# Performance work log

Measured on AMD Instinct MI355X. Metric: run time of the kernel, lower is better.

## Reference

```python
import jax, jax.numpy as jnp
import numpy as np

B, IN, FS, S, H = 4096, 4096, 4096, 64, 512  # batch, input_size, first_size, shape_lstm, n_hidden
D = FS // S  # per-step feature for left/right (=64); up/down per-step feature = S (=64)


def _lstm_cell(x, h, c, Wih, Whh, bih, bhh):
    # standard torch LSTMCell gate order: i, f, g, o
    g = x @ Wih.T + bih + h @ Whh.T + bhh  # (B, 4H)
    i, f, gg, o = jnp.split(g, 4, axis=-1)
    c = jax.nn.sigmoid(f) * c + jax.nn.sigmoid(i) * jnp.tanh(gg)
    h = jax.nn.sigmoid(o) * jnp.tanh(c)
    return h, c


def setup_inputs() -> dict:
    key = jax.random.key(0)
    ks = jax.random.split(key, 20)
    def cell(k, d_in):
        k1, k2, k3, k4 = jax.random.split(k, 4)
        s = 1.0 / np.sqrt(H)
        return (jax.random.uniform(k1, (4 * H, d_in), jnp.float32, -s, s),
                jax.random.uniform(k2, (4 * H, H), jnp.float32, -s, s),
                jax.random.uniform(k3, (4 * H,), jnp.float32, -s, s),
                jax.random.uniform(k4, (4 * H,), jnp.float32, -s, s))
    Wih_l, Whh_l, bih_l, bhh_l = cell(ks[0], D)
    Wih_r, Whh_r, bih_r, bhh_r = cell(ks[1], D)
    Wih_d, Whh_d, bih_d, bhh_d = cell(ks[2], S)
    return {
        "x": jax.random.normal(ks[3], (B, IN), jnp.float32),
        "h0": jax.random.normal(ks[4], (4, B, H), jnp.float32),
        "c0": jax.random.normal(ks[5], (4, B, H), jnp.float32),
        "W1": jax.random.normal(ks[6], (FS, IN), jnp.float32) * (1.0 / np.sqrt(IN)),
        "b1": jnp.zeros((FS,), jnp.float32),
        "Wih_l": Wih_l, "Whh_l": Whh_l, "bih_l": bih_l, "bhh_l": bhh_l,
        "Wih_r": Wih_r, "Whh_r": Whh_r, "bih_r": bih_r, "bhh_r": bhh_r,
        "Wih_d": Wih_d, "Whh_d": Whh_d, "bih_d": bih_d, "bhh_d": bhh_d,
        "W3": jax.random.normal(ks[7], (10, 4 * H), jnp.float32) * (1.0 / np.sqrt(4 * H)),
        "b3": jnp.zeros((10,), jnp.float32),
    }


def reference(x, h0, c0, W1, b1, Wih_l, Whh_l, bih_l, bhh_l,
              Wih_r, Whh_r, bih_r, bhh_r, Wih_d, Whh_d, bih_d, bhh_d, W3, b3):
    feat = jax.nn.relu(x @ W1.T + b1)            # (B, FS); dropout=identity (eval)
    il = feat.reshape(B, S, D)
    x_left = jnp.transpose(il, (1, 0, 2))         # (S, B, D)
    x_right = x_left[::-1]
    x_up = jnp.transpose(il, (2, 0, 1))           # (D, B, S); loop uses first S steps
    x_down = x_up[::-1]

    def step(carry, xs):
        (hl, cl, hr, cr, hu, cu, hd, cd) = carry
        xl, xr, xu, xd = xs
        hl, cl = _lstm_cell(xl, hl, cl, Wih_l, Whh_l, bih_l, bhh_l)
        hr, cr = _lstm_cell(xr, hr, cr, Wih_r, Whh_r, bih_r, bhh_r)
        # original code uses the DOWN cell for both up and down directions
        hu, cu = _lstm_cell(xu, hu, cu, Wih_d, Whh_d, bih_d, bhh_d)
        hd, cd = _lstm_cell(xd, hd, cd, Wih_d, Whh_d, bih_d, bhh_d)
        return (hl, cl, hr, cr, hu, cu, hd, cd), None

    carry0 = (h0[0], c0[0], h0[1], c0[1], h0[2], c0[2], h0[3], c0[3])
    (hl, _, hr, _, hu, _, hd, _), _ = jax.lax.scan(
        step, carry0, (x_left[:S], x_right[:S], x_up[:S], x_down[:S]))
    out = jnp.concatenate([hl, hr, hu, hd], axis=1)  # (B, 4H)
    logits = out @ W3.T + b3
    return jax.nn.log_softmax(logits, axis=1)
```

## Files before the change

kernel.cpp:

```cpp
#include <hip/hip_runtime.h>
#include <cstddef>
#include <cstdint>

namespace {

constexpr int kB  = 4096;
constexpr int kIN = 4096;
constexpr int kFS = 4096;
constexpr int kS  = 64;
constexpr int kH  = 512;
constexpr int kNG = 2048;
constexpr int kKC = 576;

typedef __bf16 bf16_t;
typedef __bf16 bfrag  __attribute__((ext_vector_type(8)));
typedef __bf16 bf16v4 __attribute__((ext_vector_type(4)));
typedef float  f32x4  __attribute__((ext_vector_type(4)));

__device__ __forceinline__ void gload16(const void* g, void* l) {
  __builtin_amdgcn_global_load_lds(
      (const __attribute__((address_space(1))) void*)g,
      (__attribute__((address_space(3))) void*)l, 16, 0, 0);
}

__device__ __forceinline__ float sigf(float x) { return 1.0f / (1.0f + __expf(-x)); }
__device__ __forceinline__ float tanh_fast(float x) {
  float e = __expf(2.0f * x);
  return 1.0f - 2.0f / (e + 1.0f);
}

__device__ __forceinline__ f32x4 mfma16(bfrag a, bfrag b, f32x4 c) {
  return __builtin_amdgcn_mfma_f32_16x16x32_bf16(a, b, c, 0, 0, 0);
}

__device__ __forceinline__ void vwait(const int n) {
  if (n == 6)      asm volatile("s_waitcnt vmcnt(6)" ::: "memory");
  else if (n == 4) asm volatile("s_waitcnt vmcnt(4)" ::: "memory");
  else             asm volatile("s_waitcnt vmcnt(0)" ::: "memory");
  __builtin_amdgcn_sched_barrier(0);
}


__global__ __launch_bounds__(256) void f2b4_kernel(const float* __restrict__ in,
                                                   bf16_t* __restrict__ out, int n4) {
  int i = blockIdx.x * 256 + threadIdx.x;
  if (i >= n4) return;
  float4 v = reinterpret_cast<const float4*>(in)[i];
  bf16v4 o = {(bf16_t)v.x, (bf16_t)v.y, (bf16_t)v.z, (bf16_t)v.w};
  *reinterpret_cast<bf16v4*>(out + (size_t)i * 4) = o;
}

__global__ __launch_bounds__(256) void pack_wcat_kernel(
    const float* __restrict__ Wih_l, const float* __restrict__ Whh_l,
    const float* __restrict__ Wih_r, const float* __restrict__ Whh_r,
    const float* __restrict__ Wih_d, const float* __restrict__ Whh_d,
    bf16_t* __restrict__ wcat) {
  int idx = blockIdx.x * 256 + threadIdx.x;
  if (idx >= 3 * kNG * kKC) return;
  int m = idx / (kNG * kKC);
  int rem = idx - m * (kNG * kKC);
  int rr = rem / kKC;
  int k  = rem - rr * kKC;
  int u = rr >> 2, g = rr & 3;
  int orow = g * kH + u;
  const float* Wih = (m == 0) ? Wih_l : (m == 1) ? Wih_r : Wih_d;
  const float* Whh = (m == 0) ? Whh_l : (m == 1) ? Whh_r : Whh_d;
  float v = (k < 64) ? Wih[(size_t)orow * 64 + k] : Whh[(size_t)orow * 512 + (k - 64)];
  wcat[idx] = (bf16_t)v;
}

__global__ __launch_bounds__(256) void pack_bias_kernel(
    const float* __restrict__ bih_l, const float* __restrict__ bhh_l,
    const float* __restrict__ bih_r, const float* __restrict__ bhh_r,
    const float* __restrict__ bih_d, const float* __restrict__ bhh_d,
    float* __restrict__ biasc) {
  int idx = blockIdx.x * 256 + threadIdx.x;
  if (idx >= 3 * kNG) return;
  int m = idx / kNG;
  int rr = idx - m * kNG;
  int u = rr >> 2, g = rr & 3;
  int orow = g * kH + u;
  const float* bi = (m == 0) ? bih_l : (m == 1) ? bih_r : bih_d;
  const float* bh = (m == 0) ? bhh_l : (m == 1) ? bhh_r : bhh_d;
  biasc[idx] = bi[orow] + bh[orow];
}

__global__ __launch_bounds__(256) void pack_hc_kernel(const float* __restrict__ h0,
                                                      const float* __restrict__ c0,
                                                      bf16_t* __restrict__ hbuf0,
                                                      float* __restrict__ cbuf, int n) {
  int i = blockIdx.x * 256 + threadIdx.x;
  if (i >= n) return;
  hbuf0[i] = (bf16_t)h0[i];
  cbuf[i]  = c0[i];
}

__global__ __launch_bounds__(256) void transpose64_kernel(const bf16_t* __restrict__ feat,
                                                          bf16_t* __restrict__ featT) {
  __shared__ bf16_t tile[64][65];
  const int b = blockIdx.x;
  const bf16_t* src = feat + (size_t)b * kFS;
  bf16_t* dst = featT + (size_t)b * kFS;
  for (int i = threadIdx.x; i < 4096; i += 256) tile[i >> 6][i & 63] = src[i];
  __syncthreads();
  for (int i = threadIdx.x; i < 4096; i += 256) dst[i] = tile[i & 63][i >> 6];
}


__global__ __launch_bounds__(256, 4) void gemm_feat_kernel(
    const bf16_t* __restrict__ X, const bf16_t* __restrict__ W,
    const float* __restrict__ b1, bf16_t* __restrict__ feat) {
  __shared__ bf16_t As[128 * 32];
  __shared__ bf16_t Bs[128 * 32];
  const int t = threadIdx.x;
  const int bid = blockIdx.x;
  const int widx = (bid & 7) * 128 + (bid >> 3);
  const int bm = widx & 31, bn = widx >> 5;
  const int w = t >> 6, l = t & 63;
  const int wm = (w >> 1) * 64, wn = (w & 1) * 64;
  const int sr = t >> 2;
  const int skS = ((t & 3) ^ ((t >> 3) & 3)) * 8;
  const int lr = l & 15;
  const int lkS = ((l >> 4) ^ ((l >> 1) & 3)) * 8;
  const int lrow4 = (l >> 4) * 4;

  f32x4 acc[4][4];
#pragma unroll
  for (int i = 0; i < 4; ++i)
#pragma unroll
    for (int j = 0; j < 4; ++j) acc[i][j] = (f32x4){0.f, 0.f, 0.f, 0.f};

  const bf16_t* ga = X + (size_t)(bm * 128 + sr) * kIN + skS;
  const bf16_t* gb = W + (size_t)(bn * 128 + sr) * kIN + skS;
  bf16_t* lA = As + w * 512;
  bf16_t* lB = Bs + w * 512;

  for (int kt = 0; kt < kIN / 32; ++kt) {
    gload16(ga, lA);
    gload16(ga + (size_t)64 * kIN, lA + 2048);
    gload16(gb, lB);
    gload16(gb + (size_t)64 * kIN, lB + 2048);
    ga += 32; gb += 32;
    __syncthreads();
    bfrag a[4], b[4];
#pragma unroll
    for (int mi = 0; mi < 4; ++mi)
      a[mi] = *reinterpret_cast<const bfrag*>(&As[(wm + mi * 16 + lr) * 32 + lkS]);
#pragma unroll
    for (int ni = 0; ni < 4; ++ni)
      b[ni] = *reinterpret_cast<const bfrag*>(&Bs[(wn + ni * 16 + lr) * 32 + lkS]);
#pragma unroll
    for (int mi = 0; mi < 4; ++mi)
#pragma unroll
      for (int ni = 0; ni < 4; ++ni)
        acc[mi][ni] = __builtin_amdgcn_mfma_f32_16x16x32_bf16(a[mi], b[ni], acc[mi][ni], 0, 0, 0);
    __syncthreads();
  }

#pragma unroll
  for (int ni = 0; ni < 4; ++ni) {
    const int col = bn * 128 + wn + ni * 16 + lr;
    const float bb = b1[col];
#pragma unroll
    for (int mi = 0; mi < 4; ++mi) {
#pragma unroll
      for (int r = 0; r < 4; ++r) {
        const int row = bm * 128 + wm + mi * 16 + lrow4 + r;
        float v = acc[mi][ni][r] + bb;
        feat[(size_t)row * kFS + col] = (bf16_t)fmaxf(v, 0.0f);
      }
    }
  }
}


template <class F1, class F2, class F3, class F4>
__device__ __forceinline__ void run_tile(
    const bf16_t* __restrict__ As_, const bf16_t* __restrict__ Bs_,
    f32x4 (&acc)[8][4], const int wr, const int wc, const int lr, const int lq,
    F1&& st1, F2&& st2, F3&& st3, F4&& st4,
    const int v1, const int v2, const int v3, const int v4) {
  bfrag a[8], b[8];
  const int sx = lr & 7;

#pragma unroll
  for (int mm = 0; mm < 4; ++mm)
#pragma unroll
    for (int kk = 0; kk < 2; ++kk)
      a[mm * 2 + kk] = *reinterpret_cast<const bfrag*>(
          As_ + (wr * 128 + mm * 16 + lr) * 64 + (((kk * 4 + lq) ^ sx) * 8));
#pragma unroll
  for (int nn = 0; nn < 2; ++nn)
#pragma unroll
    for (int kk = 0; kk < 2; ++kk)
      b[nn * 2 + kk] = *reinterpret_cast<const bfrag*>(
          Bs_ + (wc * 64 + nn * 16 + lr) * 64 + (((kk * 4 + lq) ^ sx) * 8));
  st1();
  __builtin_amdgcn_s_barrier();
  asm volatile("s_waitcnt lgkmcnt(0)" ::: "memory");
  __builtin_amdgcn_sched_barrier(0);
  __builtin_amdgcn_s_setprio(1);
#pragma unroll
  for (int kk = 0; kk < 2; ++kk)
#pragma unroll
    for (int mm = 0; mm < 4; ++mm)
#pragma unroll
      for (int nn = 0; nn < 2; ++nn)
        acc[mm][nn] = mfma16(a[mm * 2 + kk], b[nn * 2 + kk], acc[mm][nn]);
  __builtin_amdgcn_s_setprio(0);
  __builtin_amdgcn_sched_barrier(0);
  vwait(v1);
  __builtin_amdgcn_s_barrier();

#pragma unroll
  for (int nn = 0; nn < 2; ++nn)
#pragma unroll
    for (int kk = 0; kk < 2; ++kk)
      b[4 + nn * 2 + kk] = *reinterpret_cast<const bfrag*>(
          Bs_ + (wc * 64 + 32 + nn * 16 + lr) * 64 + (((kk * 4 + lq) ^ sx) * 8));
  st2();
  __builtin_amdgcn_s_barrier();
  asm volatile("s_waitcnt lgkmcnt(0)" ::: "memory");
  __builtin_amdgcn_sched_barrier(0);
  __builtin_amdgcn_s_setprio(1);
#pragma unroll
  for (int kk = 0; kk < 2; ++kk)
#pragma unroll
    for (int mm = 0; mm < 4; ++mm)
#pragma unroll
      for (int nn = 0; nn < 2; ++nn)
        acc[mm][2 + nn] = mfma16(a[mm * 2 + kk], b[4 + nn * 2 + kk], acc[mm][2 + nn]);
  __builtin_amdgcn_s_setprio(0);
  __builtin_amdgcn_sched_barrier(0);
  vwait(v2);
  __builtin_amdgcn_s_barrier();

#pragma unroll
  for (int mm = 0; mm < 4; ++mm)
#pragma unroll
    for (int kk = 0; kk < 2; ++kk)
      a[mm * 2 + kk] = *reinterpret_cast<const bfrag*>(
          As_ + (wr * 128 + 64 + mm * 16 + lr) * 64 + (((kk * 4 + lq) ^ sx) * 8));
  st3();
  __builtin_amdgcn_s_barrier();
  asm volatile("s_waitcnt lgkmcnt(0)" ::: "memory");
  __builtin_amdgcn_sched_barrier(0);
  __builtin_amdgcn_s_setprio(1);
#pragma unroll
  for (int kk = 0; kk < 2; ++kk)
#pragma unroll
    for (int mm = 0; mm < 4; ++mm)
#pragma unroll
      for (int nn = 0; nn < 2; ++nn)
        acc[4 + mm][nn] = mfma16(a[mm * 2 + kk], b[nn * 2 + kk], acc[4 + mm][nn]);
  __builtin_amdgcn_s_setprio(0);
  __builtin_amdgcn_sched_barrier(0);
  vwait(v3);
  __builtin_amdgcn_s_barrier();

  st4();
  __builtin_amdgcn_s_barrier();
  asm volatile("s_waitcnt lgkmcnt(0)" ::: "memory");
  __builtin_amdgcn_sched_barrier(0);
  __builtin_amdgcn_s_setprio(1);
#pragma unroll
  for (int kk = 0; kk < 2; ++kk)
#pragma unroll
    for (int mm = 0; mm < 4; ++mm)
#pragma unroll
      for (int nn = 0; nn < 2; ++nn)
        acc[4 + mm][2 + nn] = mfma16(a[mm * 2 + kk], b[4 + nn * 2 + kk], acc[4 + mm][2 + nn]);
  __builtin_amdgcn_s_setprio(0);
  __builtin_amdgcn_sched_barrier(0);
  vwait(v4);
  __builtin_amdgcn_s_barrier();
}

__global__ __launch_bounds__(512, 2) void lstm_step256_kernel(
    const bf16_t* __restrict__ feat, const bf16_t* __restrict__ featT,
    const bf16_t* __restrict__ wcat, const float* __restrict__ biasc,
    const bf16_t* __restrict__ hin, bf16_t* __restrict__ hout,
    float* __restrict__ cbuf, int s) {
  extern __shared__ __align__(16) char smem[];
  bf16_t* Ab[2] = {(bf16_t*)smem, (bf16_t*)(smem + 65536)};
  bf16_t* Bb[2] = {(bf16_t*)(smem + 32768), (bf16_t*)(smem + 98304)};

  const int t = threadIdx.x;
  const int l = t & 63, w = t >> 6;
  const int wr = w >> 2, wc = w & 3;
  const int lr = l & 15, lq = l >> 4;
  const int srow = l >> 3;
  const int sslot = (l & 7) ^ srow;

  const int bid = blockIdx.x;
  const int widx = (bid & 7) * 64 + (bid >> 3);
  const int cell = widx >> 7;
  const int rwk = widx & 127;
  const int bm = rwk >> 3, bn = rwk & 7;

  const bf16_t* xsrc = (cell < 2) ? feat : featT;
  const int off = ((cell & 1) ? (63 - s) : s) * 64;
  const int mat = (cell < 2) ? cell : 2;
  const bf16_t* Wm = wcat + (size_t)mat * kNG * kKC;
  const bf16_t* hc = hin + (size_t)cell * kB * kH;

  auto stage_A = [&](int kt, bf16_t* dstA, int ra) {
#pragma unroll
    for (int j = 0; j < 2; ++j) {
      const int row0 = ra * 64 + w * 8 + j * 128;
      bf16_t* dst = dstA + row0 * 64;
      const bf16_t* src = (kt == 0)
          ? xsrc + (size_t)(bm * 256 + row0 + srow) * kFS + off + sslot * 8
          : hc + (size_t)(bm * 256 + row0 + srow) * kH + (kt - 1) * 64 + sslot * 8;
      gload16(src, dst);
    }
  };
  auto stage_B = [&](int kt, bf16_t* dstB, int rb) {
#pragma unroll
    for (int j = 0; j < 2; ++j) {
      const int row0 = (w >> 2) * 64 + (w & 3) * 8 + rb * 32 + j * 128;
      bf16_t* dst = dstB + row0 * 64;
      const bf16_t* src =
          Wm + (size_t)(bn * 256 + row0 + srow) * kKC + kt * 64 + sslot * 8;
      gload16(src, dst);
    }
  };

  f32x4 acc[8][4];
#pragma unroll
  for (int i = 0; i < 8; ++i)
#pragma unroll
    for (int j = 0; j < 4; ++j) acc[i][j] = (f32x4){0.f, 0.f, 0.f, 0.f};

  stage_A(0, Ab[0], 0); stage_B(0, Bb[0], 0);
  stage_A(0, Ab[0], 1); stage_B(0, Bb[0], 1);
  stage_A(1, Ab[1], 0); stage_B(1, Bb[1], 0);
  vwait(4);
  __builtin_amdgcn_s_barrier();

  run_tile(Ab[0], Bb[0], acc, wr, wc, lr, lq,
           [&] { stage_A(1, Ab[1], 1); }, [&] { stage_B(1, Bb[1], 1); },
           [&] { stage_A(2, Ab[0], 0); }, [&] { stage_B(2, Bb[0], 0); },
           6, 6, 6, 6);

  for (int S = 1; S <= 5; S += 2) {
    run_tile(Ab[1], Bb[1], acc, wr, wc, lr, lq,
             [&] { stage_A(S + 1, Ab[0], 1); }, [&] { stage_B(S + 1, Bb[0], 1); },
             [&] { stage_A(S + 2, Ab[1], 0); }, [&] { stage_B(S + 2, Bb[1], 0); },
             6, 6, 6, 6);
    run_tile(Ab[0], Bb[0], acc, wr, wc, lr, lq,
             [&] { stage_A(S + 2, Ab[1], 1); }, [&] { stage_B(S + 2, Bb[1], 1); },
             [&] { stage_A(S + 3, Ab[0], 0); }, [&] { stage_B(S + 3, Bb[0], 0); },
             6, 6, 6, 6);
  }
  run_tile(Ab[1], Bb[1], acc, wr, wc, lr, lq,
           [&] { stage_A(8, Ab[0], 1); }, [&] { stage_B(8, Bb[0], 1); },
           [&] {}, [&] {}, 6, 6, 6, 4);
  run_tile(Ab[0], Bb[0], acc, wr, wc, lr, lq,
           [&] {}, [&] {}, [&] {}, [&] {}, 0, 0, 0, 0);

  float* Gw = (float*)smem + w * 2176;
  const float* biasn = biasc + mat * kNG + bn * 256 + wc * 64;
  float bb[4];
#pragma unroll
  for (int n = 0; n < 4; ++n) bb[n] = biasn[n * 16 + lr];
  const int rowg0 = bm * 256 + wr * 128;
  const int unit = bn * 64 + wc * 16 + lr;
#pragma unroll
  for (int ch = 0; ch < 4; ++ch) {
#pragma unroll
    for (int mm = 0; mm < 2; ++mm) {
      const int m = ch * 2 + mm;
#pragma unroll
      for (int n = 0; n < 4; ++n)
#pragma unroll
        for (int j = 0; j < 4; ++j)
          Gw[(mm * 16 + lq * 4 + j) * 68 + n * 16 + lr] = acc[m][n][j] + bb[n];
    }
#pragma unroll
    for (int rr = 0; rr < 8; ++rr) {
      const int row = rr * 4 + lq;
      const float4 g4 = *reinterpret_cast<const float4*>(&Gw[row * 68 + lr * 4]);
      const float iv = sigf(g4.x);
      const float fv = sigf(g4.y);
      const float gv = tanh_fast(g4.z);
      const float ov = sigf(g4.w);
      const int grow = rowg0 + ch * 32 + row;
      const size_t cidx = ((size_t)cell * kB + grow) * kH + unit;
      const float cn = fv * cbuf[cidx] + iv * gv;
      cbuf[cidx] = cn;
      hout[cidx] = (bf16_t)(ov * tanh_fast(cn));
    }
  }
}


__global__ __launch_bounds__(256) void head_kernel(const bf16_t* __restrict__ hfin,
                                                   const float* __restrict__ W3,
                                                   const float* __restrict__ b3,
                                                   float* __restrict__ out) {
  const int b = blockIdx.x, t = threadIdx.x;
  float acc[10];
#pragma unroll
  for (int j = 0; j < 10; ++j) acc[j] = 0.f;
  for (int k = t; k < 2048; k += 256) {
    const int cell = k >> 9, u = k & 511;
    const float hv = (float)hfin[((size_t)cell * kB + b) * kH + u];
#pragma unroll
    for (int j = 0; j < 10; ++j) acc[j] += hv * W3[j * 2048 + k];
  }
  __shared__ float red[256];
  __shared__ float logits[10];
  for (int j = 0; j < 10; ++j) {
    red[t] = acc[j];
    __syncthreads();
    for (int o2 = 128; o2 > 0; o2 >>= 1) {
      if (t < o2) red[t] += red[t + o2];
      __syncthreads();
    }
    if (t == 0) logits[j] = red[0] + b3[j];
    __syncthreads();
  }
  if (t == 0) {
    float mx = logits[0];
    for (int j = 1; j < 10; ++j) mx = fmaxf(mx, logits[j]);
    float se = 0.f;
    for (int j = 0; j < 10; ++j) se += expf(logits[j] - mx);
    const float lse = mx + logf(se);
    for (int j = 0; j < 10; ++j) out[(size_t)b * 10 + j] = logits[j] - lse;
  }
}

}

extern "C" void kernel_launch(void* const* d_in, const int* in_sizes, int n_in,
                              void* d_out, int out_size, void* d_ws, size_t ws_size,
                              hipStream_t stream) {
  const float* x     = (const float*)d_in[0];
  const float* h0    = (const float*)d_in[1];
  const float* c0    = (const float*)d_in[2];
  const float* W1    = (const float*)d_in[3];
  const float* b1    = (const float*)d_in[4];
  const float* Wih_l = (const float*)d_in[5];
  const float* Whh_l = (const float*)d_in[6];
  const float* bih_l = (const float*)d_in[7];
  const float* bhh_l = (const float*)d_in[8];
  const float* Wih_r = (const float*)d_in[9];
  const float* Whh_r = (const float*)d_in[10];
  const float* bih_r = (const float*)d_in[11];
  const float* bhh_r = (const float*)d_in[12];
  const float* Wih_d = (const float*)d_in[13];
  const float* Whh_d = (const float*)d_in[14];
  const float* bih_d = (const float*)d_in[15];
  const float* bhh_d = (const float*)d_in[16];
  const float* W3    = (const float*)d_in[17];
  const float* b3    = (const float*)d_in[18];
  float* out = (float*)d_out;

  char* p = (char*)d_ws;
  auto take = [&](size_t bytes) {
    char* r = p;
    p += (bytes + 255) & ~(size_t)255;
    return r;
  };
  bf16_t* xb    = (bf16_t*)take((size_t)kB * kIN * 2);
  bf16_t* w1b   = (bf16_t*)take((size_t)kFS * kIN * 2);
  bf16_t* feat  = (bf16_t*)take((size_t)kB * kFS * 2);
  bf16_t* wcat  = (bf16_t*)take((size_t)3 * kNG * kKC * 2);
  float*  biasc = (float*)take((size_t)3 * kNG * 4);
  float*  cbuf  = (float*)take((size_t)4 * kB * kH * 4);
  bf16_t* featT = xb;
  bf16_t* hbuf  = w1b;
  const size_t HSZ = (size_t)4 * kB * kH;

  (void)hipFuncSetAttribute(reinterpret_cast<const void*>(&lstm_step256_kernel),
                            hipFuncAttributeMaxDynamicSharedMemorySize, 131072);

  f2b4_kernel<<<(kB * kIN / 4) / 256, 256, 0, stream>>>(x, xb, kB * kIN / 4);
  f2b4_kernel<<<(kFS * kIN / 4) / 256, 256, 0, stream>>>(W1, w1b, kFS * kIN / 4);
  gemm_feat_kernel<<<dim3(1024), 256, 0, stream>>>(xb, w1b, b1, feat);
  transpose64_kernel<<<kB, 256, 0, stream>>>(feat, featT);
  pack_wcat_kernel<<<(3 * kNG * kKC + 255) / 256, 256, 0, stream>>>(
      Wih_l, Whh_l, Wih_r, Whh_r, Wih_d, Whh_d, wcat);
  pack_bias_kernel<<<(3 * kNG + 255) / 256, 256, 0, stream>>>(
      bih_l, bhh_l, bih_r, bhh_r, bih_d, bhh_d, biasc);
  pack_hc_kernel<<<(int)(HSZ / 256), 256, 0, stream>>>(h0, c0, hbuf, cbuf, (int)HSZ);

  for (int s = 0; s < 64; ++s) {
    lstm_step256_kernel<<<dim3(512), 512, 131072, stream>>>(
        feat, featT, wcat, biasc,
        hbuf + (size_t)(s & 1) * HSZ, hbuf + (size_t)((s + 1) & 1) * HSZ, cbuf, s);
  }
  head_kernel<<<kB, 256, 0, stream>>>(hbuf, W3, b3, out);
}
```

Before: 4.151 ms.

## Double-buffer register fragments to overlap LDS reads with MFMA in LSTM GEMM

Restructures the per-tile MFMA schedule so LDS fragment reads for the next quadrant (and the next tile's first A/B fragments) are issued before the current quadrant's MFMAs. The per-quadrant lgkmcnt(0) waits and extra barriers are dropped, so LDS latency can hide behind matrix math. The vmcnt schedule for the tail tiles is adjusted to match. This costs more fragment registers (aP/aQ/bP/bQ), which could cause spills at the launch bound of 512 threads with 2 blocks per CU, and makes the buffer-reuse ordering harder to get right.

```diff
diff --git a/kernel.cpp b/kernel.cpp
--- a/kernel.cpp
+++ b/kernel.cpp
@@ -33,9 +33,10 @@
   return __builtin_amdgcn_mfma_f32_16x16x32_bf16(a, b, c, 0, 0, 0);
 }
 
-__device__ __forceinline__ void vwait(const int n) {
+__device__ __forceinline__ void vwait(int n) {
   if (n == 6)      asm volatile("s_waitcnt vmcnt(6)" ::: "memory");
   else if (n == 4) asm volatile("s_waitcnt vmcnt(4)" ::: "memory");
+  else if (n == 2) asm volatile("s_waitcnt vmcnt(2)" ::: "memory");
   else             asm volatile("s_waitcnt vmcnt(0)" ::: "memory");
   __builtin_amdgcn_sched_barrier(0);
 }
@@ -174,107 +175,12 @@
 }
 
 
-template <class F1, class F2, class F3, class F4>
-__device__ __forceinline__ void run_tile(
-    const bf16_t* __restrict__ As_, const bf16_t* __restrict__ Bs_,
-    f32x4 (&acc)[8][4], const int wr, const int wc, const int lr, const int lq,
-    F1&& st1, F2&& st2, F3&& st3, F4&& st4,
-    const int v1, const int v2, const int v3, const int v4) {
-  bfrag a[8], b[8];
-  const int sx = lr & 7;
-
-#pragma unroll
-  for (int mm = 0; mm < 4; ++mm)
-#pragma unroll
-    for (int kk = 0; kk < 2; ++kk)
-      a[mm * 2 + kk] = *reinterpret_cast<const bfrag*>(
-          As_ + (wr * 128 + mm * 16 + lr) * 64 + (((kk * 4 + lq) ^ sx) * 8));
-#pragma unroll
-  for (int nn = 0; nn < 2; ++nn)
-#pragma unroll
-    for (int kk = 0; kk < 2; ++kk)
-      b[nn * 2 + kk] = *reinterpret_cast<const bfrag*>(
-          Bs_ + (wc * 64 + nn * 16 + lr) * 64 + (((kk * 4 + lq) ^ sx) * 8));
-  st1();
-  __builtin_amdgcn_s_barrier();
-  asm volatile("s_waitcnt lgkmcnt(0)" ::: "memory");
-  __builtin_amdgcn_sched_barrier(0);
-  __builtin_amdgcn_s_setprio(1);
-#pragma unroll
-  for (int kk = 0; kk < 2; ++kk)
-#pragma unroll
-    for (int mm = 0; mm < 4; ++mm)
-#pragma unroll
-      for (int nn = 0; nn < 2; ++nn)
-        acc[mm][nn] = mfma16(a[mm * 2 + kk], b[nn * 2 + kk], acc[mm][nn]);
-  __builtin_amdgcn_s_setprio(0);
-  __builtin_amdgcn_sched_barrier(0);
-  vwait(v1);
-  __builtin_amdgcn_s_barrier();
-
-#pragma unroll
-  for (int nn = 0; nn < 2; ++nn)
-#pragma unroll
-    for (int kk = 0; kk < 2; ++kk)
-      b[4 + nn * 2 + kk] = *reinterpret_cast<const bfrag*>(
-          Bs_ + (wc * 64 + 32 + nn * 16 + lr) * 64 + (((kk * 4 + lq) ^ sx) * 8));
-  st2();
-  __builtin_amdgcn_s_barrier();
-  asm volatile("s_waitcnt lgkmcnt(0)" ::: "memory");
-  __builtin_amdgcn_sched_barrier(0);
-  __builtin_amdgcn_s_setprio(1);
-#pragma unroll
-  for (int kk = 0; kk < 2; ++kk)
-#pragma unroll
-    for (int mm = 0; mm < 4; ++mm)
-#pragma unroll
-      for (int nn = 0; nn < 2; ++nn)
-        acc[mm][2 + nn] = mfma16(a[mm * 2 + kk], b[4 + nn * 2 + kk], acc[mm][2 + nn]);
-  __builtin_amdgcn_s_setprio(0);
-  __builtin_amdgcn_sched_barrier(0);
-  vwait(v2);
-  __builtin_amdgcn_s_barrier();
-
-#pragma unroll
-  for (int mm = 0; mm < 4; ++mm)
-#pragma unroll
-    for (int kk = 0; kk < 2; ++kk)
-      a[mm * 2 + kk] = *reinterpret_cast<const bfrag*>(
-          As_ + (wr * 128 + 64 + mm * 16 + lr) * 64 + (((kk * 4 + lq) ^ sx) * 8));
-  st3();
-  __builtin_amdgcn_s_barrier();
-  asm volatile("s_waitcnt lgkmcnt(0)" ::: "memory");
-  __builtin_amdgcn_sched_barrier(0);
-  __builtin_amdgcn_s_setprio(1);
-#pragma unroll
-  for (int kk = 0; kk < 2; ++kk)
-#pragma unroll
-    for (int mm = 0; mm < 4; ++mm)
-#pragma unroll
-      for (int nn = 0; nn < 2; ++nn)
-        acc[4 + mm][nn] = mfma16(a[mm * 2 + kk], b[nn * 2 + kk], acc[4 + mm][nn]);
-  __builtin_amdgcn_s_setprio(0);
-  __builtin_amdgcn_sched_barrier(0);
-  vwait(v3);
-  __builtin_amdgcn_s_barrier();
-
-  st4();
-  __builtin_amdgcn_s_barrier();
-  asm volatile("s_waitcnt lgkmcnt(0)" ::: "memory");
-  __builtin_amdgcn_sched_barrier(0);
-  __builtin_amdgcn_s_setprio(1);
-#pragma unroll
-  for (int kk = 0; kk < 2; ++kk)
-#pragma unroll
-    for (int mm = 0; mm < 4; ++mm)
-#pragma unroll
-      for (int nn = 0; nn < 2; ++nn)
-        acc[4 + mm][2 + nn] = mfma16(a[mm * 2 + kk], b[4 + nn * 2 + kk], acc[4 + mm][2 + nn]);
-  __builtin_amdgcn_s_setprio(0);
-  __builtin_amdgcn_sched_barrier(0);
-  vwait(v4);
-  __builtin_amdgcn_s_barrier();
-}
+#define QUAD(A, B, MO, NO)                                              \
+  _Pragma("unroll") for (int kk = 0; kk < 2; ++kk)                      \
+  _Pragma("unroll") for (int mm = 0; mm < 4; ++mm)                      \
+  _Pragma("unroll") for (int nn = 0; nn < 2; ++nn)                      \
+      acc[(MO) + mm][(NO) + nn] =                                       \
+          mfma16(A[mm * 2 + kk], B[nn * 2 + kk], acc[(MO) + mm][(NO) + nn]);
 
 __global__ __launch_bounds__(512, 2) void lstm_step256_kernel(
     const bf16_t* __restrict__ feat, const bf16_t* __restrict__ featT,
@@ -282,13 +188,12 @@
     const bf16_t* __restrict__ hin, bf16_t* __restrict__ hout,
     float* __restrict__ cbuf, int s) {
   extern __shared__ __align__(16) char smem[];
-  bf16_t* Ab[2] = {(bf16_t*)smem, (bf16_t*)(smem + 65536)};
-  bf16_t* Bb[2] = {(bf16_t*)(smem + 32768), (bf16_t*)(smem + 98304)};
 
   const int t = threadIdx.x;
   const int l = t & 63, w = t >> 6;
   const int wr = w >> 2, wc = w & 3;
   const int lr = l & 15, lq = l >> 4;
+  const int sx = lr & 7;
   const int srow = l >> 3;
   const int sslot = (l & 7) ^ srow;
 
@@ -298,28 +203,31 @@
   const int rwk = widx & 127;
   const int bm = rwk >> 3, bn = rwk & 7;
 
+  auto Abase = [&](int i) -> bf16_t* { return (bf16_t*)(smem + i * 65536); };
+  auto Bbase = [&](int i) -> bf16_t* { return (bf16_t*)(smem + 32768 + i * 65536); };
+
   const bf16_t* xsrc = (cell < 2) ? feat : featT;
   const int off = ((cell & 1) ? (63 - s) : s) * 64;
   const int mat = (cell < 2) ? cell : 2;
   const bf16_t* Wm = wcat + (size_t)mat * kNG * kKC;
   const bf16_t* hc = hin + (size_t)cell * kB * kH;
 
-  auto stage_A = [&](int kt, bf16_t* dstA, int ra) {
+  auto stage_A = [&](int kt, int buf, int ra) {
 #pragma unroll
     for (int j = 0; j < 2; ++j) {
       const int row0 = ra * 64 + w * 8 + j * 128;
-      bf16_t* dst = dstA + row0 * 64;
+      bf16_t* dst = Abase(buf) + row0 * 64;
       const bf16_t* src = (kt == 0)
           ? xsrc + (size_t)(bm * 256 + row0 + srow) * kFS + off + sslot * 8
           : hc + (size_t)(bm * 256 + row0 + srow) * kH + (kt - 1) * 64 + sslot * 8;
       gload16(src, dst);
     }
   };
-  auto stage_B = [&](int kt, bf16_t* dstB, int rb) {
+  auto stage_B = [&](int kt, int buf, int rb) {
 #pragma unroll
     for (int j = 0; j < 2; ++j) {
       const int row0 = (w >> 2) * 64 + (w & 3) * 8 + rb * 32 + j * 128;
-      bf16_t* dst = dstB + row0 * 64;
+      bf16_t* dst = Bbase(buf) + row0 * 64;
       const bf16_t* src =
           Wm + (size_t)(bn * 256 + row0 + srow) * kKC + kt * 64 + sslot * 8;
       gload16(src, dst);
@@ -332,32 +240,81 @@
 #pragma unroll
     for (int j = 0; j < 4; ++j) acc[i][j] = (f32x4){0.f, 0.f, 0.f, 0.f};
 
-  stage_A(0, Ab[0], 0); stage_B(0, Bb[0], 0);
-  stage_A(0, Ab[0], 1); stage_B(0, Bb[0], 1);
-  stage_A(1, Ab[1], 0); stage_B(1, Bb[1], 0);
+  bfrag aP[8], aQ[8], bP[4], bQ[4];
+
+  auto read_a = [&](bfrag (&d)[8], int buf, int mh) {
+    const bf16_t* base = Abase(buf);
+#pragma unroll
+    for (int mm = 0; mm < 4; ++mm)
+#pragma unroll
+      for (int kk = 0; kk < 2; ++kk)
+        d[mm * 2 + kk] = *reinterpret_cast<const bfrag*>(
+            base + (wr * 128 + mh * 64 + mm * 16 + lr) * 64 + (((kk * 4 + lq) ^ sx) * 8));
+  };
+  auto read_b = [&](bfrag (&d)[4], int buf, int nh) {
+    const bf16_t* base = Bbase(buf);
+#pragma unroll
+    for (int nn = 0; nn < 2; ++nn)
+#pragma unroll
+      for (int kk = 0; kk < 2; ++kk)
+        d[nn * 2 + kk] = *reinterpret_cast<const bfrag*>(
+            base + (wc * 64 + nh * 32 + nn * 16 + lr) * 64 + (((kk * 4 + lq) ^ sx) * 8));
+  };
+
+  auto tile = [&](int tt, int v1, int v2, int v3, int v4, bool s12, bool s34, bool r34) {
+    const int cur = tt & 1, nxt = cur ^ 1;
+    read_b(bQ, cur, 1);
+    if (s12) stage_B(tt + 1, nxt, 1);
+    __builtin_amdgcn_sched_barrier(0);
+    __builtin_amdgcn_s_setprio(1);
+    QUAD(aP, bP, 0, 0);
+    __builtin_amdgcn_s_setprio(0);
+    __builtin_amdgcn_sched_barrier(0);
+    vwait(v1);
+    __builtin_amdgcn_s_barrier();
+    read_a(aQ, cur, 1);
+    if (s12) stage_A(tt + 1, nxt, 1);
+    __builtin_amdgcn_sched_barrier(0);
+    __builtin_amdgcn_s_setprio(1);
+    QUAD(aP, bQ, 0, 2);
+    __builtin_amdgcn_s_setprio(0);
+    __builtin_amdgcn_sched_barrier(0);
+    vwait(v2);
+    __builtin_amdgcn_s_barrier();
+    if (r34) read_a(aP, nxt, 0);
+    if (s34) stage_A(tt + 2, cur, 0);
+    __builtin_amdgcn_sched_barrier(0);
+    __builtin_amdgcn_s_setprio(1);
+    QUAD(aQ, bP, 4, 0);
+    __builtin_amdgcn_s_setprio(0);
+    __builtin_amdgcn_sched_barrier(0);
+    vwait(v3);
+    __builtin_amdgcn_s_barrier();
+    if (r34) read_b(bP, nxt, 0);
+    if (s34) stage_B(tt + 2, cur, 0);
+    __builtin_amdgcn_sched_barrier(0);
+    __builtin_amdgcn_s_setprio(1);
+    QUAD(aQ, bQ, 4, 2);
+    __builtin_amdgcn_s_setprio(0);
+    __builtin_amdgcn_sched_barrier(0);
+    vwait(v4);
+    __builtin_amdgcn_s_barrier();
+  };
+
+  stage_A(0, 0, 0); stage_B(0, 0, 0);
+  stage_A(0, 0, 1); stage_B(0, 0, 1);
+  stage_A(1, 1, 0); stage_B(1, 1, 0);
   vwait(4);
   __builtin_amdgcn_s_barrier();
-
-  run_tile(Ab[0], Bb[0], acc, wr, wc, lr, lq,
-           [&] { stage_A(1, Ab[1], 1); }, [&] { stage_B(1, Bb[1], 1); },
-           [&] { stage_A(2, Ab[0], 0); }, [&] { stage_B(2, Bb[0], 0); },
-           6, 6, 6, 6);
-
-  for (int S = 1; S <= 5; S += 2) {
-    run_tile(Ab[1], Bb[1], acc, wr, wc, lr, lq,
-             [&] { stage_A(S + 1, Ab[0], 1); }, [&] { stage_B(S + 1, Bb[0], 1); },
-             [&] { stage_A(S + 2, Ab[1], 0); }, [&] { stage_B(S + 2, Bb[1], 0); },
-             6, 6, 6, 6);
-    run_tile(Ab[0], Bb[0], acc, wr, wc, lr, lq,
-             [&] { stage_A(S + 2, Ab[1], 1); }, [&] { stage_B(S + 2, Bb[1], 1); },
-             [&] { stage_A(S + 3, Ab[0], 0); }, [&] { stage_B(S + 3, Bb[0], 0); },
-             6, 6, 6, 6);
-  }
-  run_tile(Ab[1], Bb[1], acc, wr, wc, lr, lq,
-           [&] { stage_A(8, Ab[0], 1); }, [&] { stage_B(8, Bb[0], 1); },
-           [&] {}, [&] {}, 6, 6, 6, 4);
-  run_tile(Ab[0], Bb[0], acc, wr, wc, lr, lq,
-           [&] {}, [&] {}, [&] {}, [&] {}, 0, 0, 0, 0);
+  read_a(aP, 0, 0);
+  read_b(bP, 0, 0);
+
+  for (int tt = 0; tt < 7; ++tt)
+    tile(tt, 6, 6, 6, 6, true, true, true);
+  tile(7, 6, 6, 4, 2, true, false, true);
+  tile(8, 0, 0, 0, 0, false, false, false);
+
+  __syncthreads();
 
   float* Gw = (float*)smem + w * 2176;
   const float* biasn = biasc + mat * kNG + bn * 256 + wc * 64;
```

Measured after the change: 4.533 ms. 1.09x slower.
